# Kernel tuning notes

Measured on AMD Instinct MI355X. Metric: run time of the kernel, lower is better.

Reference implementation:

```python
import jax, jax.numpy as jnp
import numpy as np

TOTAL_NODES = 10000
E_OLD = 320000
E_NEW = 320000


def setup_inputs() -> dict:
    key = jax.random.key(0)
    k1, k2, k3, k4, k5 = jax.random.split(key, 5)
    edge_index_old = jax.random.randint(k1, (2, E_OLD), 0, TOTAL_NODES, dtype=jnp.int32)
    # Make new edges overlap old edges for half of E_new so both the
    # retained-edge and new-edge branches are exercised.
    rand_new = jax.random.randint(k2, (2, E_NEW), 0, TOTAL_NODES, dtype=jnp.int32)
    half = E_NEW // 2
    edge_index_new = jnp.concatenate([edge_index_old[:, :half], rand_new[:, half:]], axis=1)
    edge_attr_old = jax.random.normal(k3, (E_OLD, 3), dtype=jnp.float32)
    flow_old = jax.random.normal(k4, (E_OLD, 1), dtype=jnp.float32)
    edge_attr_new = jax.random.normal(k5, (E_NEW, 3), dtype=jnp.float32)
    return {
        "edge_index_old": edge_index_old,
        "edge_attr_old": edge_attr_old,
        "flow_old": flow_old,
        "edge_index_new": edge_index_new,
        "edge_attr_new": edge_attr_new,
        "total_nodes": TOTAL_NODES,
    }


def reference(edge_index_old, edge_attr_old, flow_old, edge_index_new, edge_attr_new, total_nodes):
    dtype = edge_attr_new.dtype
    E_old = edge_attr_old.shape[0]
    # key(src, dst) = src * total_nodes + dst  (unique per node pair)
    old_keys = edge_index_old[0] * total_nodes + edge_index_old[1]  # [E_old] int32
    new_keys = edge_index_new[0] * total_nodes + edge_index_new[1]  # [E_new] int32
    # Dense scatter-built lookup table of size total_nodes^2 (the memory hog).
    table = jnp.full((total_nodes * total_nodes,), -1, dtype=jnp.int32)
    table = table.at[old_keys].set(jnp.arange(E_old, dtype=jnp.int32))
    match_idx = table[new_keys]                    # [E_new], -1 if no match
    retained = match_idx >= 0                      # [E_new] bool
    old_feats = jnp.concatenate([edge_attr_old, flow_old], axis=-1)  # [E_old, 4]
    gathered = old_feats[jnp.where(retained, match_idx, 0)]          # [E_new, 4]
    aligned_old = jnp.where(retained[:, None], gathered, jnp.zeros((), dtype=dtype))
    is_new_edge = (~retained).astype(dtype)[:, None]                 # [E_new, 1]
    return jnp.concatenate([aligned_old, edge_attr_new, is_new_edge], axis=-1)  # [E_new, 8]
```

## Files before the change

### kernel.cpp

```cpp
#include <hip/hip_runtime.h>


#define EMPTY_SLOT 0xAAAAAAAAAAAAAAAAull
#define EMPTY_KEY  0xAAAAAAAAu

typedef float vfloat4 __attribute__((ext_vector_type(4)));

__device__ __forceinline__ unsigned hash_key(unsigned key, unsigned mask) {
    unsigned h = key * 2654435761u;
    h ^= h >> 16;
    return h & mask;
}

__global__ void __launch_bounds__(512)
insert_kernel(const int* __restrict__ ei_old, int E_old,
              const float* __restrict__ attr_old,
              const float* __restrict__ flow_old,
              const int* __restrict__ total_nodes_p,
              unsigned long long* __restrict__ slots,
              vfloat4* __restrict__ feats,
              unsigned mask) {
    int e = blockIdx.x * blockDim.x + threadIdx.x;
    if (e >= E_old) return;

    vfloat4 f;
    f.x = __builtin_nontemporal_load(&attr_old[3 * e + 0]);
    f.y = __builtin_nontemporal_load(&attr_old[3 * e + 1]);
    f.z = __builtin_nontemporal_load(&attr_old[3 * e + 2]);
    f.w = __builtin_nontemporal_load(&flow_old[e]);
    feats[e] = f;

    const int tn  = *total_nodes_p;
    const int src = __builtin_nontemporal_load(&ei_old[e]);
    const int dst = __builtin_nontemporal_load(&ei_old[E_old + e]);
    const unsigned key = (unsigned)(src * tn + dst);
    const unsigned long long desired =
        ((unsigned long long)(unsigned)e << 32) | key;

    unsigned h = hash_key(key, mask);
    for (;;) {
        unsigned long long old = atomicCAS(&slots[h], EMPTY_SLOT, desired);
        if (old == EMPTY_SLOT) return;
        if ((unsigned)old == key) {
            atomicMax(&slots[h], desired);
            return;
        }
        h = (h + 1) & mask;
    }
}

__global__ void __launch_bounds__(512)
align_kernel(const int* __restrict__ ei_new, int E_new,
             const vfloat4* __restrict__ feats,
             const float* __restrict__ attr_new,
             const int* __restrict__ total_nodes_p,
             const unsigned long long* __restrict__ slots,
             unsigned mask, float* __restrict__ out) {
    int e = blockIdx.x * blockDim.x + threadIdx.x;
    if (e >= E_new) return;
    const int tn  = *total_nodes_p;
    const int src = __builtin_nontemporal_load(&ei_new[e]);
    const int dst = __builtin_nontemporal_load(&ei_new[E_new + e]);
    const unsigned key = (unsigned)(src * tn + dst);

    unsigned h = hash_key(key, mask);
    int m = -1;
    for (;;) {
        unsigned long long cur = slots[h];
        unsigned ck = (unsigned)cur;
        if (ck == key) { m = (int)(cur >> 32); break; }
        if (ck == EMPTY_KEY) break;
        h = (h + 1) & mask;
    }

    vfloat4 a, b;
    if (m >= 0) {
        a = feats[m];
        b.w = 0.0f;
    } else {
        a = (vfloat4){0.f, 0.f, 0.f, 0.f};
        b.w = 1.0f;
    }
    b.x = __builtin_nontemporal_load(&attr_new[3 * e + 0]);
    b.y = __builtin_nontemporal_load(&attr_new[3 * e + 1]);
    b.z = __builtin_nontemporal_load(&attr_new[3 * e + 2]);

    vfloat4* o = (vfloat4*)(out + 8 * (size_t)e);
    __builtin_nontemporal_store(a, &o[0]);
    __builtin_nontemporal_store(b, &o[1]);
}

extern "C" void kernel_launch(void* const* d_in, const int* in_sizes, int n_in,
                              void* d_out, int out_size, void* d_ws, size_t ws_size,
                              hipStream_t stream) {
    const int*   ei_old   = (const int*)  d_in[0];
    const float* attr_old = (const float*)d_in[1];
    const float* flow_old = (const float*)d_in[2];
    const int*   ei_new   = (const int*)  d_in[3];
    const float* attr_new = (const float*)d_in[4];
    const int*   tn_p     = (const int*)  d_in[5];

    const int E_old = in_sizes[0] / 2;
    const int E_new = in_sizes[3] / 2;

    size_t slots_n = 1u << 20;
    while (slots_n * 8 + (size_t)E_old * 16 > ws_size && slots_n > (1u << 19))
        slots_n >>= 1;
    unsigned mask = (unsigned)slots_n - 1;

    unsigned long long* slots = (unsigned long long*)d_ws;
    vfloat4* feats = (vfloat4*)((char*)d_ws + slots_n * 8);

    const int B = 512;
    insert_kernel<<<(E_old + B - 1) / B, B, 0, stream>>>(
        ei_old, E_old, attr_old, flow_old, tn_p, slots, feats, mask);
    align_kernel<<<(E_new + B - 1) / B, B, 0, stream>>>(
        ei_new, E_new, feats, attr_new, tn_p, slots, mask, (float*)d_out);
}
```

Before: 105.2 us.

## Fuse hash insert and lookup into one cooperative persistent kernel

Merges the hash-table insert kernel and the align/lookup kernel into a single cooperative kernel. The two phases run as grid-stride loops separated by a grid-wide sync. This is meant to remove the second kernel launch and the gap between launches. In exchange it adds grid.sync overhead, uses a capped grid size that may limit parallelism, and queries device properties and occupancy on the host for every launch.

```diff
diff --git a/kernel.cpp b/kernel.cpp
--- a/kernel.cpp
+++ b/kernel.cpp
@@ -1,4 +1,7 @@
 #include <hip/hip_runtime.h>
+#include <hip/hip_cooperative_groups.h>
+
+namespace cg = cooperative_groups;
 
 
 #define EMPTY_SLOT 0xAAAAAAAAAAAAAAAAull
@@ -12,82 +15,80 @@
     return h & mask;
 }
 
-__global__ void __launch_bounds__(512)
-insert_kernel(const int* __restrict__ ei_old, int E_old,
-              const float* __restrict__ attr_old,
-              const float* __restrict__ flow_old,
-              const int* __restrict__ total_nodes_p,
-              unsigned long long* __restrict__ slots,
-              vfloat4* __restrict__ feats,
-              unsigned mask) {
-    int e = blockIdx.x * blockDim.x + threadIdx.x;
-    if (e >= E_old) return;
-
-    vfloat4 f;
-    f.x = __builtin_nontemporal_load(&attr_old[3 * e + 0]);
-    f.y = __builtin_nontemporal_load(&attr_old[3 * e + 1]);
-    f.z = __builtin_nontemporal_load(&attr_old[3 * e + 2]);
-    f.w = __builtin_nontemporal_load(&flow_old[e]);
-    feats[e] = f;
-
-    const int tn  = *total_nodes_p;
-    const int src = __builtin_nontemporal_load(&ei_old[e]);
-    const int dst = __builtin_nontemporal_load(&ei_old[E_old + e]);
-    const unsigned key = (unsigned)(src * tn + dst);
-    const unsigned long long desired =
-        ((unsigned long long)(unsigned)e << 32) | key;
-
-    unsigned h = hash_key(key, mask);
-    for (;;) {
-        unsigned long long old = atomicCAS(&slots[h], EMPTY_SLOT, desired);
-        if (old == EMPTY_SLOT) return;
-        if ((unsigned)old == key) {
-            atomicMax(&slots[h], desired);
-            return;
-        }
-        h = (h + 1) & mask;
-    }
-}
-
-__global__ void __launch_bounds__(512)
-align_kernel(const int* __restrict__ ei_new, int E_new,
-             const vfloat4* __restrict__ feats,
+__global__ void __launch_bounds__(256, 4)
+fused_kernel(const int* __restrict__ ei_old, int E_old,
+             const float* __restrict__ attr_old,
+             const float* __restrict__ flow_old,
+             const int* __restrict__ ei_new, int E_new,
              const float* __restrict__ attr_new,
              const int* __restrict__ total_nodes_p,
-             const unsigned long long* __restrict__ slots,
+             unsigned long long* __restrict__ slots,
+             vfloat4* __restrict__ feats,
              unsigned mask, float* __restrict__ out) {
-    int e = blockIdx.x * blockDim.x + threadIdx.x;
-    if (e >= E_new) return;
+    cg::grid_group grid = cg::this_grid();
+    const int nth = (int)(gridDim.x * blockDim.x);
+    const int tid = (int)(blockIdx.x * blockDim.x + threadIdx.x);
     const int tn  = *total_nodes_p;
-    const int src = __builtin_nontemporal_load(&ei_new[e]);
-    const int dst = __builtin_nontemporal_load(&ei_new[E_new + e]);
-    const unsigned key = (unsigned)(src * tn + dst);
 
-    unsigned h = hash_key(key, mask);
-    int m = -1;
-    for (;;) {
-        unsigned long long cur = slots[h];
-        unsigned ck = (unsigned)cur;
-        if (ck == key) { m = (int)(cur >> 32); break; }
-        if (ck == EMPTY_KEY) break;
-        h = (h + 1) & mask;
+    for (int e = tid; e < E_old; e += nth) {
+        vfloat4 f;
+        f.x = __builtin_nontemporal_load(&attr_old[3 * e + 0]);
+        f.y = __builtin_nontemporal_load(&attr_old[3 * e + 1]);
+        f.z = __builtin_nontemporal_load(&attr_old[3 * e + 2]);
+        f.w = __builtin_nontemporal_load(&flow_old[e]);
+        feats[e] = f;
+
+        const int src = __builtin_nontemporal_load(&ei_old[e]);
+        const int dst = __builtin_nontemporal_load(&ei_old[E_old + e]);
+        const unsigned key = (unsigned)(src * tn + dst);
+        const unsigned long long desired =
+            ((unsigned long long)(unsigned)e << 32) | key;
+
+        unsigned h = hash_key(key, mask);
+        for (;;) {
+            unsigned long long old = atomicCAS(&slots[h], EMPTY_SLOT, desired);
+            if (old == EMPTY_SLOT) break;
+            if ((unsigned)old == key) {
+                atomicMax(&slots[h], desired);
+                break;
+            }
+            h = (h + 1) & mask;
+        }
     }
 
-    vfloat4 a, b;
-    if (m >= 0) {
-        a = feats[m];
-        b.w = 0.0f;
-    } else {
-        a = (vfloat4){0.f, 0.f, 0.f, 0.f};
-        b.w = 1.0f;
+    grid.sync();
+
+    for (int e = tid; e < E_new; e += nth) {
+        const int src = __builtin_nontemporal_load(&ei_new[e]);
+        const int dst = __builtin_nontemporal_load(&ei_new[E_new + e]);
+        const unsigned key = (unsigned)(src * tn + dst);
+
+        unsigned h = hash_key(key, mask);
+        int m = -1;
+        for (;;) {
+            unsigned long long cur = slots[h];
+            unsigned ck = (unsigned)cur;
+            if (ck == key) { m = (int)(cur >> 32); break; }
+            if (ck == EMPTY_KEY) break;
+            h = (h + 1) & mask;
+        }
+
+        vfloat4 a, b;
+        if (m >= 0) {
+            a = feats[m];
+            b.w = 0.0f;
+        } else {
+            a = (vfloat4){0.f, 0.f, 0.f, 0.f};
+            b.w = 1.0f;
+        }
+        b.x = __builtin_nontemporal_load(&attr_new[3 * e + 0]);
+        b.y = __builtin_nontemporal_load(&attr_new[3 * e + 1]);
+        b.z = __builtin_nontemporal_load(&attr_new[3 * e + 2]);
+
+        vfloat4* o = (vfloat4*)(out + 8 * (size_t)e);
+        __builtin_nontemporal_store(a, &o[0]);
+        __builtin_nontemporal_store(b, &o[1]);
     }
-    b.x = __builtin_nontemporal_load(&attr_new[3 * e + 0]);
-    b.y = __builtin_nontemporal_load(&attr_new[3 * e + 1]);
-    b.z = __builtin_nontemporal_load(&attr_new[3 * e + 2]);
-
-    vfloat4* o = (vfloat4*)(out + 8 * (size_t)e);
-    __builtin_nontemporal_store(a, &o[0]);
-    __builtin_nontemporal_store(b, &o[1]);
 }
 
 extern "C" void kernel_launch(void* const* d_in, const int* in_sizes, int n_in,
@@ -100,8 +101,8 @@
     const float* attr_new = (const float*)d_in[4];
     const int*   tn_p     = (const int*)  d_in[5];
 
-    const int E_old = in_sizes[0] / 2;
-    const int E_new = in_sizes[3] / 2;
+    int E_old = in_sizes[0] / 2;
+    int E_new = in_sizes[3] / 2;
 
     size_t slots_n = 1u << 20;
     while (slots_n * 8 + (size_t)E_old * 16 > ws_size && slots_n > (1u << 19))
@@ -110,10 +111,24 @@
 
     unsigned long long* slots = (unsigned long long*)d_ws;
     vfloat4* feats = (vfloat4*)((char*)d_ws + slots_n * 8);
+    float* out = (float*)d_out;
 
-    const int B = 512;
-    insert_kernel<<<(E_old + B - 1) / B, B, 0, stream>>>(
-        ei_old, E_old, attr_old, flow_old, tn_p, slots, feats, mask);
-    align_kernel<<<(E_new + B - 1) / B, B, 0, stream>>>(
-        ei_new, E_new, feats, attr_new, tn_p, slots, mask, (float*)d_out);
+    int blk_per_cu = 4;
+    (void)hipOccupancyMaxActiveBlocksPerMultiprocessor(
+        &blk_per_cu, (const void*)fused_kernel, 256, 0);
+    if (blk_per_cu > 4) blk_per_cu = 4;
+    if (blk_per_cu < 1) blk_per_cu = 1;
+    hipDeviceProp_t prop;
+    int dev = 0;
+    hipGetDevice(&dev);
+    hipGetDeviceProperties(&prop, dev);
+    int grid = prop.multiProcessorCount * blk_per_cu;
+    if (grid > 1024) grid = 1024;
+
+    void* args[] = {(void*)&ei_old, (void*)&E_old, (void*)&attr_old,
+                    (void*)&flow_old, (void*)&ei_new, (void*)&E_new,
+                    (void*)&attr_new, (void*)&tn_p, (void*)&slots,
+                    (void*)&feats, (void*)&mask, (void*)&out};
+    hipLaunchCooperativeKernel((void*)fused_kernel, dim3(grid), dim3(256),
+                               args, 0, stream);
 }
```

Result: slower. 230.0 us (+118.6%).
